# Kernel optimization log

Measured on AMD Instinct MI355X. Metric: run time of the kernel, lower is better.

Reference implementation:

```python
import jax, jax.numpy as jnp
import numpy as np
import math

TOTAL_RANK = 16
ACTIVE_RANK = 8
HADAMARD_DIM = 16
ADAPT_DIM = 32
HIDDEN = 2048
LN_EPS = 1e-5


def _hadamard(n: int) -> np.ndarray:
    # Replicates the module's recursive construction (normalizes by sqrt(n) at EVERY level).
    if n == 1:
        return np.array([[1.0]], dtype=np.float32)
    h = _hadamard(n // 2)
    return (np.block([[h, h], [h, -h]]) / math.sqrt(n)).astype(np.float32)


def setup_inputs() -> dict:
    key = jax.random.key(0)
    ks = jax.random.split(key, 8)
    B, S = 8, 4096
    hidden_states = jax.random.normal(ks[0], (B, S, HIDDEN), dtype=jnp.float32)
    rank_activations = jax.random.normal(ks[1], (B, S, TOTAL_RANK), dtype=jnp.float32)
    W1 = jax.random.normal(ks[2], (HIDDEN, ADAPT_DIM), dtype=jnp.float32) / math.sqrt(HIDDEN)
    b1 = jnp.zeros((ADAPT_DIM,), dtype=jnp.float32)
    ln_gamma = jnp.ones((ADAPT_DIM,), dtype=jnp.float32)
    ln_beta = jnp.zeros((ADAPT_DIM,), dtype=jnp.float32)
    W2 = jax.random.normal(ks[3], (ADAPT_DIM, TOTAL_RANK), dtype=jnp.float32) / math.sqrt(ADAPT_DIM)
    b2 = jnp.zeros((TOTAL_RANK,), dtype=jnp.float32)
    mask_logits = jax.random.normal(ks[4], (TOTAL_RANK,), dtype=jnp.float32) * 0.1
    rank_scales = jnp.ones((TOTAL_RANK,), dtype=jnp.float32)
    return {
        "hidden_states": hidden_states,
        "rank_activations": rank_activations,
        "W1": W1, "b1": b1, "ln_gamma": ln_gamma, "ln_beta": ln_beta,
        "W2": W2, "b2": b2, "mask_logits": mask_logits, "rank_scales": rank_scales,
    }


def reference(hidden_states, rank_activations, W1, b1, ln_gamma, ln_beta, W2, b2,
              mask_logits, rank_scales):
    B = hidden_states.shape[0]
    # Instance-adaptive logits: adaptation_net(hidden.mean(dim=1)) — eval mode (dropout off).
    pooled = jnp.mean(hidden_states, axis=1)                      # [B, H]
    x = pooled @ W1 + b1                                          # [B, A]
    mu = jnp.mean(x, axis=-1, keepdims=True)
    var = jnp.var(x, axis=-1, keepdims=True)
    x = (x - mu) * jax.lax.rsqrt(var + LN_EPS) * ln_gamma + ln_beta
    x = jax.nn.gelu(x, approximate=False)
    instance_logits = x @ W2 + b2                                 # [B, R]
    combined = instance_logits + mask_logits[None, :]
    # k-hot mask via top-k + scatter (eval path)
    _, idx = jax.lax.top_k(combined, ACTIVE_RANK)                 # [B, k]
    mask = jnp.zeros_like(combined).at[jnp.arange(B)[:, None], idx].set(1.0)
    # mask + scale
    scaled = rank_activations * mask[:, None, :] * rank_scales[None, None, :]  # [B,S,R]
    # Hadamard path: total_rank == hadamard_dim == 16 -> no padding, slice is no-op.
    H = jnp.asarray(_hadamard(HADAMARD_DIM))
    transformed = jnp.einsum('bsr,dr->bsd', scaled, H)            # x @ H.T
    final = transformed[:, :, :TOTAL_RANK]
    return final
```

## Files before the change

kernel.cpp:

```cpp
#include <hip/hip_runtime.h>
#include <hip/hip_bf16.h>
#include <math.h>

#define S_LEN   4096
#define HID     2048
#define NB      8
#define SC      128
#define S_PER   (S_LEN / SC)
#define R       16
#define AD      32

typedef float f4 __attribute__((ext_vector_type(4)));

__global__ void pool_proj(const float* __restrict__ hs,
                          const float* __restrict__ W1,
                          float* __restrict__ xpart) {
    __shared__ float hsum[HID];
    __shared__ float cpart[8][AD];
    int t  = threadIdx.x;
    int sc = blockIdx.x;
    int b  = blockIdx.y;

    const float* base = hs + ((size_t)b * S_LEN + (size_t)sc * S_PER) * HID;
    const f4* p0 = (const f4*)(base + t * 4);
    const f4* p1 = (const f4*)(base + 1024 + t * 4);
    f4 a0 = (f4)(0.f);
    f4 a1 = (f4)(0.f);
#pragma unroll 8
    for (int s = 0; s < S_PER; ++s) {
        f4 v0 = __builtin_nontemporal_load(p0 + (size_t)s * (HID / 4));
        f4 v1 = __builtin_nontemporal_load(p1 + (size_t)s * (HID / 4));
        a0 += v0;
        a1 += v1;
    }
    *(f4*)&hsum[t * 4]        = a0;
    *(f4*)&hsum[1024 + t * 4] = a1;
    __syncthreads();

    int j = t & 31, g = t >> 5;
    const float* w = W1 + (size_t)(g * 256) * AD + j;
    float c = 0.f;
#pragma unroll 4
    for (int k = 0; k < 256; ++k)
        c += hsum[g * 256 + k] * w[(size_t)k * AD];
    cpart[g][j] = c;
    __syncthreads();

    if (t < AD) {
        float s = 0.f;
#pragma unroll
        for (int gg = 0; gg < 8; ++gg) s += cpart[gg][t];
        xpart[((size_t)(b * SC + sc)) * AD + t] = s;
    }
}

__global__ void ctrl_hadamard(const float* __restrict__ xpart,
                              const float* __restrict__ b1,
                              const float* __restrict__ gamma,
                              const float* __restrict__ beta,
                              const float* __restrict__ W2,
                              const float* __restrict__ b2v,
                              const float* __restrict__ mlog,
                              const float* __restrict__ rsc,
                              const float* __restrict__ ra,
                              float* __restrict__ out) {
    __shared__ float xp[4][AD];
    __shared__ float xv[AD];
    __shared__ float xg[AD];
    __shared__ float comb[R];
    __shared__ float ms[R];
    int t   = threadIdx.x;
    int blk = blockIdx.x;
    int b   = blk >> 5;

    int j = t & 31, g = t >> 5;
    const float* xb = xpart + (size_t)b * SC * AD;
    float s = 0.f;
#pragma unroll 8
    for (int r = 0; r < 32; ++r) s += xb[(size_t)(g * 32 + r) * AD + j];
    xp[g][j] = s;
    __syncthreads();

    if (t < AD) {
        float x = 0.f;
#pragma unroll
        for (int gg = 0; gg < 4; ++gg) x += xp[gg][t];
        xv[t] = x * (1.0f / (float)S_LEN) + b1[t];
    }
    __syncthreads();

    if (t < AD) {
        float mu = 0.f;
#pragma unroll
        for (int k = 0; k < AD; ++k) mu += xv[k];
        mu *= (1.0f / AD);
        float var = 0.f;
#pragma unroll
        for (int k = 0; k < AD; ++k) { float d = xv[k] - mu; var += d * d; }
        var *= (1.0f / AD);
        float x = (xv[t] - mu) * rsqrtf(var + 1e-5f) * gamma[t] + beta[t];
        xg[t] = 0.5f * x * (1.0f + erff(x * 0.70710678118654752f));
    }
    __syncthreads();

    if (t < R) {
        float lg = b2v[t];
#pragma unroll
        for (int k = 0; k < AD; ++k) lg += xg[k] * W2[(size_t)k * R + t];
        comb[t] = lg + mlog[t];
    }
    __syncthreads();

    if (t < R) {
        float v = comb[t];
        int cnt = 0;
#pragma unroll
        for (int k = 0; k < R; ++k)
            cnt += (comb[k] > v) || (comb[k] == v && k < t);
        ms[t] = (cnt < 8) ? rsc[t] : 0.f;
    }
    __syncthreads();

    size_t row = (size_t)blk * 128 + t;
    const f4* src = (const f4*)(ra + row * R);
    float a[R];
#pragma unroll
    for (int i = 0; i < 4; ++i) {
        f4 v = __builtin_nontemporal_load(src + i);
        a[4 * i + 0] = v.x; a[4 * i + 1] = v.y;
        a[4 * i + 2] = v.z; a[4 * i + 3] = v.w;
    }
#pragma unroll
    for (int r = 0; r < R; ++r) a[r] *= ms[r];

#pragma unroll
    for (int hstep = 1; hstep < R; hstep <<= 1) {
#pragma unroll
        for (int i = 0; i < R; ++i) {
            if ((i & hstep) == 0) {
                float u = a[i], v = a[i | hstep];
                a[i] = u + v; a[i | hstep] = u - v;
            }
        }
    }

    f4* dst = (f4*)(out + row * R);
#pragma unroll
    for (int i = 0; i < 4; ++i) {
        f4 v;
        v.x = a[4 * i + 0] * 0.03125f; v.y = a[4 * i + 1] * 0.03125f;
        v.z = a[4 * i + 2] * 0.03125f; v.w = a[4 * i + 3] * 0.03125f;
        __builtin_nontemporal_store(v, dst + i);
    }
}

extern "C" void kernel_launch(void* const* d_in, const int* in_sizes, int n_in,
                              void* d_out, int out_size, void* d_ws, size_t ws_size,
                              hipStream_t stream) {
    const float* hs    = (const float*)d_in[0];
    const float* ra    = (const float*)d_in[1];
    const float* W1    = (const float*)d_in[2];
    const float* b1    = (const float*)d_in[3];
    const float* gamma = (const float*)d_in[4];
    const float* beta  = (const float*)d_in[5];
    const float* W2    = (const float*)d_in[6];
    const float* b2v   = (const float*)d_in[7];
    const float* mlog  = (const float*)d_in[8];
    const float* rsc   = (const float*)d_in[9];
    float* out = (float*)d_out;

    float* xpart = (float*)d_ws;

    pool_proj    <<<dim3(SC, NB), 256, 0, stream>>>(hs, W1, xpart);
    ctrl_hadamard<<<256, 128, 0, stream>>>(xpart, b1, gamma, beta,
                                           W2, b2v, mlog, rsc, ra, out);
}
```

Measured before the change: 56.85 us.

## Fuse pooling and controller/Hadamard into one cooperative kernel with grid sync

Merges the two kernels into a single cooperative launch of 1024 blocks. A grid-wide sync separates the pooled projection partials from the per-batch controller and the Hadamard stage. Each block then redoes the small controller computation and transforms 32 rows using only one wave. This is meant to remove the second launch and the gap between kernels. In exchange it adds grid-sync cost, requires all 1024 blocks to be co-resident, and leaves most threads idle in the Hadamard phase.

```diff
diff --git a/kernel.cpp b/kernel.cpp
--- a/kernel.cpp
+++ b/kernel.cpp
@@ -1,4 +1,5 @@
 #include <hip/hip_runtime.h>
+#include <hip/hip_cooperative_groups.h>
 #include <hip/hip_bf16.h>
 #include <math.h>
 
@@ -12,145 +13,152 @@
 
 typedef float f4 __attribute__((ext_vector_type(4)));
 
-__global__ void pool_proj(const float* __restrict__ hs,
-                          const float* __restrict__ W1,
-                          float* __restrict__ xpart) {
+namespace cg = cooperative_groups;
+
+__global__ __launch_bounds__(256, 4)
+void fused_all(const float* __restrict__ hs,
+               const float* __restrict__ W1,
+               const float* __restrict__ b1,
+               const float* __restrict__ gamma,
+               const float* __restrict__ beta,
+               const float* __restrict__ W2,
+               const float* __restrict__ b2v,
+               const float* __restrict__ mlog,
+               const float* __restrict__ rsc,
+               const float* __restrict__ ra,
+               float* __restrict__ xpart,
+               float* __restrict__ out) {
     __shared__ float hsum[HID];
-    __shared__ float cpart[8][AD];
-    int t  = threadIdx.x;
-    int sc = blockIdx.x;
-    int b  = blockIdx.y;
-
-    const float* base = hs + ((size_t)b * S_LEN + (size_t)sc * S_PER) * HID;
-    const f4* p0 = (const f4*)(base + t * 4);
-    const f4* p1 = (const f4*)(base + 1024 + t * 4);
-    f4 a0 = (f4)(0.f);
-    f4 a1 = (f4)(0.f);
-#pragma unroll 8
-    for (int s = 0; s < S_PER; ++s) {
-        f4 v0 = __builtin_nontemporal_load(p0 + (size_t)s * (HID / 4));
-        f4 v1 = __builtin_nontemporal_load(p1 + (size_t)s * (HID / 4));
-        a0 += v0;
-        a1 += v1;
-    }
-    *(f4*)&hsum[t * 4]        = a0;
-    *(f4*)&hsum[1024 + t * 4] = a1;
-    __syncthreads();
-
-    int j = t & 31, g = t >> 5;
-    const float* w = W1 + (size_t)(g * 256) * AD + j;
-    float c = 0.f;
-#pragma unroll 4
-    for (int k = 0; k < 256; ++k)
-        c += hsum[g * 256 + k] * w[(size_t)k * AD];
-    cpart[g][j] = c;
-    __syncthreads();
-
-    if (t < AD) {
-        float s = 0.f;
-#pragma unroll
-        for (int gg = 0; gg < 8; ++gg) s += cpart[gg][t];
-        xpart[((size_t)(b * SC + sc)) * AD + t] = s;
-    }
-}
-
-__global__ void ctrl_hadamard(const float* __restrict__ xpart,
-                              const float* __restrict__ b1,
-                              const float* __restrict__ gamma,
-                              const float* __restrict__ beta,
-                              const float* __restrict__ W2,
-                              const float* __restrict__ b2v,
-                              const float* __restrict__ mlog,
-                              const float* __restrict__ rsc,
-                              const float* __restrict__ ra,
-                              float* __restrict__ out) {
-    __shared__ float xp[4][AD];
+    __shared__ float gp[8][AD];
     __shared__ float xv[AD];
     __shared__ float xg[AD];
     __shared__ float comb[R];
     __shared__ float ms[R];
+
     int t   = threadIdx.x;
     int blk = blockIdx.x;
-    int b   = blk >> 5;
+    int b   = blk >> 7;
 
-    int j = t & 31, g = t >> 5;
-    const float* xb = xpart + (size_t)b * SC * AD;
-    float s = 0.f;
+    {
+        int sc = blk & (SC - 1);
+        const float* base = hs + ((size_t)b * S_LEN + (size_t)sc * S_PER) * HID;
+        const f4* p0 = (const f4*)(base + t * 4);
+        const f4* p1 = (const f4*)(base + 1024 + t * 4);
+        f4 a0 = (f4)(0.f);
+        f4 a1 = (f4)(0.f);
 #pragma unroll 8
-    for (int r = 0; r < 32; ++r) s += xb[(size_t)(g * 32 + r) * AD + j];
-    xp[g][j] = s;
-    __syncthreads();
+        for (int s = 0; s < S_PER; ++s) {
+            f4 v0 = __builtin_nontemporal_load(p0 + (size_t)s * (HID / 4));
+            f4 v1 = __builtin_nontemporal_load(p1 + (size_t)s * (HID / 4));
+            a0 += v0;
+            a1 += v1;
+        }
+        *(f4*)&hsum[t * 4]        = a0;
+        *(f4*)&hsum[1024 + t * 4] = a1;
+        __syncthreads();
 
-    if (t < AD) {
-        float x = 0.f;
+        int j = t & 31, g = t >> 5;
+        const float* w = W1 + (size_t)(g * 256) * AD + j;
+        float c = 0.f;
+#pragma unroll 4
+        for (int k = 0; k < 256; ++k)
+            c += hsum[g * 256 + k] * w[(size_t)k * AD];
+        gp[g][j] = c;
+        __syncthreads();
+
+        if (t < AD) {
+            float s = 0.f;
 #pragma unroll
-        for (int gg = 0; gg < 4; ++gg) x += xp[gg][t];
-        xv[t] = x * (1.0f / (float)S_LEN) + b1[t];
-    }
-    __syncthreads();
-
-    if (t < AD) {
-        float mu = 0.f;
-#pragma unroll
-        for (int k = 0; k < AD; ++k) mu += xv[k];
-        mu *= (1.0f / AD);
-        float var = 0.f;
-#pragma unroll
-        for (int k = 0; k < AD; ++k) { float d = xv[k] - mu; var += d * d; }
-        var *= (1.0f / AD);
-        float x = (xv[t] - mu) * rsqrtf(var + 1e-5f) * gamma[t] + beta[t];
-        xg[t] = 0.5f * x * (1.0f + erff(x * 0.70710678118654752f));
-    }
-    __syncthreads();
-
-    if (t < R) {
-        float lg = b2v[t];
-#pragma unroll
-        for (int k = 0; k < AD; ++k) lg += xg[k] * W2[(size_t)k * R + t];
-        comb[t] = lg + mlog[t];
-    }
-    __syncthreads();
-
-    if (t < R) {
-        float v = comb[t];
-        int cnt = 0;
-#pragma unroll
-        for (int k = 0; k < R; ++k)
-            cnt += (comb[k] > v) || (comb[k] == v && k < t);
-        ms[t] = (cnt < 8) ? rsc[t] : 0.f;
-    }
-    __syncthreads();
-
-    size_t row = (size_t)blk * 128 + t;
-    const f4* src = (const f4*)(ra + row * R);
-    float a[R];
-#pragma unroll
-    for (int i = 0; i < 4; ++i) {
-        f4 v = __builtin_nontemporal_load(src + i);
-        a[4 * i + 0] = v.x; a[4 * i + 1] = v.y;
-        a[4 * i + 2] = v.z; a[4 * i + 3] = v.w;
-    }
-#pragma unroll
-    for (int r = 0; r < R; ++r) a[r] *= ms[r];
-
-#pragma unroll
-    for (int hstep = 1; hstep < R; hstep <<= 1) {
-#pragma unroll
-        for (int i = 0; i < R; ++i) {
-            if ((i & hstep) == 0) {
-                float u = a[i], v = a[i | hstep];
-                a[i] = u + v; a[i | hstep] = u - v;
-            }
+            for (int gg = 0; gg < 8; ++gg) s += gp[gg][t];
+            xpart[((size_t)blk) * AD + t] = s;
         }
     }
 
-    f4* dst = (f4*)(out + row * R);
+    cg::this_grid().sync();
+
+    {
+        int j = t & 31, g = t >> 5;
+        const float* xb = xpart + (size_t)b * SC * AD;
+        float s = 0.f;
+#pragma unroll 4
+        for (int r = 0; r < 16; ++r)
+            s += xb[(size_t)(g * 16 + r) * AD + j];
+        gp[g][j] = s;
+        __syncthreads();
+
+        if (t < AD) {
+            float x = 0.f;
 #pragma unroll
-    for (int i = 0; i < 4; ++i) {
-        f4 v;
-        v.x = a[4 * i + 0] * 0.03125f; v.y = a[4 * i + 1] * 0.03125f;
-        v.z = a[4 * i + 2] * 0.03125f; v.w = a[4 * i + 3] * 0.03125f;
-        __builtin_nontemporal_store(v, dst + i);
+            for (int gg = 0; gg < 8; ++gg) x += gp[gg][t];
+            xv[t] = x * (1.0f / (float)S_LEN) + b1[t];
+        }
+        __syncthreads();
+
+        if (t < AD) {
+            float mu = 0.f;
+#pragma unroll
+            for (int k = 0; k < AD; ++k) mu += xv[k];
+            mu *= (1.0f / AD);
+            float var = 0.f;
+#pragma unroll
+            for (int k = 0; k < AD; ++k) { float d = xv[k] - mu; var += d * d; }
+            var *= (1.0f / AD);
+            float x = (xv[t] - mu) * rsqrtf(var + 1e-5f) * gamma[t] + beta[t];
+            xg[t] = 0.5f * x * (1.0f + erff(x * 0.70710678118654752f));
+        }
+        __syncthreads();
+
+        if (t < R) {
+            float lg = b2v[t];
+#pragma unroll
+            for (int k = 0; k < AD; ++k) lg += xg[k] * W2[(size_t)k * R + t];
+            comb[t] = lg + mlog[t];
+        }
+        __syncthreads();
+
+        if (t < R) {
+            float v = comb[t];
+            int cnt = 0;
+#pragma unroll
+            for (int k = 0; k < R; ++k)
+                cnt += (comb[k] > v) || (comb[k] == v && k < t);
+            ms[t] = (cnt < 8) ? rsc[t] : 0.f;
+        }
+        __syncthreads();
+    }
+
+    if (t < 32) {
+        size_t row = (size_t)blk * 32 + t;
+        const f4* src = (const f4*)(ra + row * R);
+        float a[R];
+#pragma unroll
+        for (int i = 0; i < 4; ++i) {
+            f4 v = __builtin_nontemporal_load(src + i);
+            a[4 * i + 0] = v.x; a[4 * i + 1] = v.y;
+            a[4 * i + 2] = v.z; a[4 * i + 3] = v.w;
+        }
+#pragma unroll
+        for (int r = 0; r < R; ++r) a[r] *= ms[r];
+
+#pragma unroll
+        for (int hstep = 1; hstep < R; hstep <<= 1) {
+#pragma unroll
+            for (int i = 0; i < R; ++i) {
+                if ((i & hstep) == 0) {
+                    float u = a[i], v = a[i | hstep];
+                    a[i] = u + v; a[i | hstep] = u - v;
+                }
+            }
+        }
+
+        f4* dst = (f4*)(out + row * R);
+#pragma unroll
+        for (int i = 0; i < 4; ++i) {
+            f4 v;
+            v.x = a[4 * i + 0] * 0.03125f; v.y = a[4 * i + 1] * 0.03125f;
+            v.z = a[4 * i + 2] * 0.03125f; v.w = a[4 * i + 3] * 0.03125f;
+            __builtin_nontemporal_store(v, dst + i);
+        }
     }
 }
 
@@ -167,11 +175,14 @@
     const float* b2v   = (const float*)d_in[7];
     const float* mlog  = (const float*)d_in[8];
     const float* rsc   = (const float*)d_in[9];
-    float* out = (float*)d_out;
-
+    float* out   = (float*)d_out;
     float* xpart = (float*)d_ws;
 
-    pool_proj    <<<dim3(SC, NB), 256, 0, stream>>>(hs, W1, xpart);
-    ctrl_hadamard<<<256, 128, 0, stream>>>(xpart, b1, gamma, beta,
-                                           W2, b2v, mlog, rsc, ra, out);
+    void* args[] = {
+        (void*)&hs, (void*)&W1, (void*)&b1, (void*)&gamma, (void*)&beta,
+        (void*)&W2, (void*)&b2v, (void*)&mlog, (void*)&rsc, (void*)&ra,
+        (void*)&xpart, (void*)&out
+    };
+    hipLaunchCooperativeKernel((void*)fused_all, dim3(NB * SC), dim3(256),
+                               args, 0, stream);
 }
```

After: 202.9 us. 3.57x slower.

## Replace shared-memory controller stages with per-wave shuffle reductions

Applied to the files above, without the earlier changes.

Rewrites the per-block controller (pooled sum, LayerNorm, GELU, W2 projection, top-k mask) so each 64-lane wave computes it redundantly with cross-lane shuffles, removing the shared-memory stages and block barriers. The output scale of 1/32 is folded into the mask values, and the rank_activations load becomes a regular rather than nontemporal load. This cuts serial latency before the streaming Hadamard part, at the cost of some redundant arithmetic per wave.

```diff
diff --git a/kernel.cpp b/kernel.cpp
--- a/kernel.cpp
+++ b/kernel.cpp
@@ -64,74 +64,92 @@
                               const float* __restrict__ rsc,
                               const float* __restrict__ ra,
                               float* __restrict__ out) {
-    __shared__ float xp[4][AD];
-    __shared__ float xv[AD];
-    __shared__ float xg[AD];
-    __shared__ float comb[R];
-    __shared__ float ms[R];
     int t   = threadIdx.x;
     int blk = blockIdx.x;
     int b   = blk >> 5;
+    int lane = t & 63;
+    int j    = lane & 31;
+    int half = lane >> 5;
 
-    int j = t & 31, g = t >> 5;
-    const float* xb = xpart + (size_t)b * SC * AD;
+    const float* xb = xpart + ((size_t)b * SC + half * 64) * AD + j;
     float s = 0.f;
 #pragma unroll 8
-    for (int r = 0; r < 32; ++r) s += xb[(size_t)(g * 32 + r) * AD + j];
-    xp[g][j] = s;
-    __syncthreads();
+    for (int r = 0; r < 64; ++r) s += xb[(size_t)r * AD];
+    s += __shfl_xor(s, 32);
 
-    if (t < AD) {
-        float x = 0.f;
+    float xv = s * (1.0f / (float)S_LEN) + b1[j];
+
+    float m = xv;
 #pragma unroll
-        for (int gg = 0; gg < 4; ++gg) x += xp[gg][t];
-        xv[t] = x * (1.0f / (float)S_LEN) + b1[t];
+    for (int d = 1; d < 64; d <<= 1) m += __shfl_xor(m, d);
+    float mu = m * (1.0f / 64.0f);
+    float dv = xv - mu;
+    float vs = dv * dv;
+#pragma unroll
+    for (int d = 1; d < 64; d <<= 1) vs += __shfl_xor(vs, d);
+    float var = vs * (1.0f / 64.0f);
+
+    float xln = dv * rsqrtf(var + 1e-5f) * gamma[j] + beta[j];
+    float xg  = 0.5f * xln * (1.0f + erff(xln * 0.70710678118654752f));
+
+    float p[8];
+#pragma unroll
+    for (int kk = 0; kk < 8; ++kk)
+        p[kk] = xg * W2[(size_t)j * R + half * 8 + kk];
+#pragma unroll
+    for (int d = 1; d < 32; d <<= 1) {
+#pragma unroll
+        for (int kk = 0; kk < 8; ++kk) p[kk] += __shfl_xor(p[kk], d);
     }
-    __syncthreads();
+#pragma unroll
+    for (int kk = 0; kk < 8; ++kk)
+        p[kk] += b2v[half * 8 + kk] + mlog[half * 8 + kk];
 
-    if (t < AD) {
-        float mu = 0.f;
+    float q[8];
 #pragma unroll
-        for (int k = 0; k < AD; ++k) mu += xv[k];
-        mu *= (1.0f / AD);
-        float var = 0.f;
+    for (int kk = 0; kk < 8; ++kk) q[kk] = __shfl_xor(p[kk], 32);
+    float lo[8], hi[8];
 #pragma unroll
-        for (int k = 0; k < AD; ++k) { float d = xv[k] - mu; var += d * d; }
-        var *= (1.0f / AD);
-        float x = (xv[t] - mu) * rsqrtf(var + 1e-5f) * gamma[t] + beta[t];
-        xg[t] = 0.5f * x * (1.0f + erff(x * 0.70710678118654752f));
+    for (int kk = 0; kk < 8; ++kk) {
+        lo[kk] = (half == 0) ? p[kk] : q[kk];
+        hi[kk] = (half == 0) ? q[kk] : p[kk];
     }
-    __syncthreads();
 
-    if (t < R) {
-        float lg = b2v[t];
+    float msv[R];
 #pragma unroll
-        for (int k = 0; k < AD; ++k) lg += xg[k] * W2[(size_t)k * R + t];
-        comb[t] = lg + mlog[t];
-    }
-    __syncthreads();
-
-    if (t < R) {
-        float v = comb[t];
+    for (int k = 0; k < 8; ++k) {
+        float v = lo[k];
         int cnt = 0;
 #pragma unroll
-        for (int k = 0; k < R; ++k)
-            cnt += (comb[k] > v) || (comb[k] == v && k < t);
-        ms[t] = (cnt < 8) ? rsc[t] : 0.f;
+        for (int m2 = 0; m2 < 8; ++m2) {
+            cnt += (lo[m2] > v) || (lo[m2] == v && m2 < k);
+            cnt += (hi[m2] > v);
+        }
+        msv[k] = (cnt < 8) ? rsc[k] * 0.03125f : 0.f;
     }
-    __syncthreads();
+#pragma unroll
+    for (int k = 0; k < 8; ++k) {
+        float v = hi[k];
+        int cnt = 0;
+#pragma unroll
+        for (int m2 = 0; m2 < 8; ++m2) {
+            cnt += (lo[m2] > v) || (lo[m2] == v);
+            cnt += (hi[m2] > v) || (hi[m2] == v && m2 < k);
+        }
+        msv[8 + k] = (cnt < 8) ? rsc[8 + k] * 0.03125f : 0.f;
+    }
 
     size_t row = (size_t)blk * 128 + t;
     const f4* src = (const f4*)(ra + row * R);
     float a[R];
 #pragma unroll
     for (int i = 0; i < 4; ++i) {
-        f4 v = __builtin_nontemporal_load(src + i);
+        f4 v = src[i];
         a[4 * i + 0] = v.x; a[4 * i + 1] = v.y;
         a[4 * i + 2] = v.z; a[4 * i + 3] = v.w;
     }
 #pragma unroll
-    for (int r = 0; r < R; ++r) a[r] *= ms[r];
+    for (int r = 0; r < R; ++r) a[r] *= msv[r];
 
 #pragma unroll
     for (int hstep = 1; hstep < R; hstep <<= 1) {
@@ -148,8 +166,8 @@
 #pragma unroll
     for (int i = 0; i < 4; ++i) {
         f4 v;
-        v.x = a[4 * i + 0] * 0.03125f; v.y = a[4 * i + 1] * 0.03125f;
-        v.z = a[4 * i + 2] * 0.03125f; v.w = a[4 * i + 3] * 0.03125f;
+        v.x = a[4 * i + 0]; v.y = a[4 * i + 1];
+        v.z = a[4 * i + 2]; v.w = a[4 * i + 3];
         __builtin_nontemporal_store(v, dst + i);
     }
 }
```

After: 60.46 us. 1.06x slower.

## Move controller MLP into last-arriving pool block via atomic counter

Applied to the files above, without the earlier changes.

Instead of every Hadamard block redundantly reducing 128 partials and running LayerNorm, GELU, the W2 projection and top-k, the last pool_proj block per batch (found through an atomic counter) does this once and writes a per-batch mask with the 1/32 scale folded in. The Hadamard kernel then only loads 16 mask values and uses 256-thread blocks. This adds a memset launch and a threadfence/atomic handshake, and the tail block runs serially after the last arrival.

```diff
diff --git a/kernel.cpp b/kernel.cpp
--- a/kernel.cpp
+++ b/kernel.cpp
@@ -14,9 +14,22 @@
 
 __global__ void pool_proj(const float* __restrict__ hs,
                           const float* __restrict__ W1,
-                          float* __restrict__ xpart) {
+                          const float* __restrict__ b1,
+                          const float* __restrict__ gamma,
+                          const float* __restrict__ beta,
+                          const float* __restrict__ W2,
+                          const float* __restrict__ b2v,
+                          const float* __restrict__ mlog,
+                          const float* __restrict__ rsc,
+                          float* __restrict__ xpart,
+                          float* __restrict__ msout,
+                          int* __restrict__ cnt) {
     __shared__ float hsum[HID];
     __shared__ float cpart[8][AD];
+    __shared__ float xv[AD];
+    __shared__ float xg[AD];
+    __shared__ float comb[R];
+    __shared__ int   iswin;
     int t  = threadIdx.x;
     int sc = blockIdx.x;
     int b  = blockIdx.y;
@@ -52,40 +65,36 @@
         for (int gg = 0; gg < 8; ++gg) s += cpart[gg][t];
         xpart[((size_t)(b * SC + sc)) * AD + t] = s;
     }
-}
-
-__global__ void ctrl_hadamard(const float* __restrict__ xpart,
-                              const float* __restrict__ b1,
-                              const float* __restrict__ gamma,
-                              const float* __restrict__ beta,
-                              const float* __restrict__ W2,
-                              const float* __restrict__ b2v,
-                              const float* __restrict__ mlog,
-                              const float* __restrict__ rsc,
-                              const float* __restrict__ ra,
-                              float* __restrict__ out) {
-    __shared__ float xp[4][AD];
-    __shared__ float xv[AD];
-    __shared__ float xg[AD];
-    __shared__ float comb[R];
-    __shared__ float ms[R];
-    int t   = threadIdx.x;
-    int blk = blockIdx.x;
-    int b   = blk >> 5;
-
-    int j = t & 31, g = t >> 5;
-    const float* xb = xpart + (size_t)b * SC * AD;
-    float s = 0.f;
-#pragma unroll 8
-    for (int r = 0; r < 32; ++r) s += xb[(size_t)(g * 32 + r) * AD + j];
-    xp[g][j] = s;
-    __syncthreads();
-
-    if (t < AD) {
-        float x = 0.f;
-#pragma unroll
-        for (int gg = 0; gg < 4; ++gg) x += xp[gg][t];
-        xv[t] = x * (1.0f / (float)S_LEN) + b1[t];
+
+    if (t == 0) {
+        __threadfence();
+        int old = atomicAdd(&cnt[b], 1);
+        iswin = (old == SC - 1);
+        if (iswin) __threadfence();
+    }
+    __syncthreads();
+    if (!iswin) return;
+
+    {
+        f4* red = (f4*)hsum;
+        const f4* xp4 = (const f4*)(xpart + (size_t)b * SC * AD);
+        int c4 = t & 7, rg = t >> 3;
+        f4 acc = (f4)(0.f);
+#pragma unroll
+        for (int r = 0; r < 4; ++r)
+            acc += xp4[(size_t)(rg + r * 32) * 8 + c4];
+        red[rg * 8 + c4] = acc;
+    }
+    __syncthreads();
+    if (t < 8) {
+        f4* red = (f4*)hsum;
+        f4 s = (f4)(0.f);
+#pragma unroll
+        for (int rg = 0; rg < 32; ++rg) s += red[rg * 8 + t];
+        xv[t * 4 + 0] = s.x * (1.0f / (float)S_LEN) + b1[t * 4 + 0];
+        xv[t * 4 + 1] = s.y * (1.0f / (float)S_LEN) + b1[t * 4 + 1];
+        xv[t * 4 + 2] = s.z * (1.0f / (float)S_LEN) + b1[t * 4 + 2];
+        xv[t * 4 + 3] = s.w * (1.0f / (float)S_LEN) + b1[t * 4 + 3];
     }
     __syncthreads();
 
@@ -113,15 +122,25 @@
 
     if (t < R) {
         float v = comb[t];
-        int cnt = 0;
+        int cn = 0;
 #pragma unroll
         for (int k = 0; k < R; ++k)
-            cnt += (comb[k] > v) || (comb[k] == v && k < t);
-        ms[t] = (cnt < 8) ? rsc[t] : 0.f;
-    }
-    __syncthreads();
-
-    size_t row = (size_t)blk * 128 + t;
+            cn += (comb[k] > v) || (comb[k] == v && k < t);
+        msout[b * R + t] = (cn < 8) ? rsc[t] * 0.03125f : 0.f;
+    }
+}
+
+__global__ void apply_hadamard(const float* __restrict__ msout,
+                               const float* __restrict__ ra,
+                               float* __restrict__ out) {
+    __shared__ float ms[R];
+    int t   = threadIdx.x;
+    int blk = blockIdx.x;
+    int b   = blk >> 4;
+    if (t < R) ms[t] = msout[b * R + t];
+    __syncthreads();
+
+    size_t row = (size_t)blk * 256 + t;
     const f4* src = (const f4*)(ra + row * R);
     float a[R];
 #pragma unroll
@@ -148,8 +167,8 @@
 #pragma unroll
     for (int i = 0; i < 4; ++i) {
         f4 v;
-        v.x = a[4 * i + 0] * 0.03125f; v.y = a[4 * i + 1] * 0.03125f;
-        v.z = a[4 * i + 2] * 0.03125f; v.w = a[4 * i + 3] * 0.03125f;
+        v.x = a[4 * i + 0]; v.y = a[4 * i + 1];
+        v.z = a[4 * i + 2]; v.w = a[4 * i + 3];
         __builtin_nontemporal_store(v, dst + i);
     }
 }
@@ -170,8 +189,12 @@
     float* out = (float*)d_out;
 
     float* xpart = (float*)d_ws;
-
-    pool_proj    <<<dim3(SC, NB), 256, 0, stream>>>(hs, W1, xpart);
-    ctrl_hadamard<<<256, 128, 0, stream>>>(xpart, b1, gamma, beta,
-                                           W2, b2v, mlog, rsc, ra, out);
+    float* msout = xpart + (size_t)NB * SC * AD;
+    int*   cnt   = (int*)(msout + NB * R);
+
+    hipMemsetAsync(cnt, 0, NB * sizeof(int), stream);
+    pool_proj     <<<dim3(SC, NB), 256, 0, stream>>>(hs, W1, b1, gamma, beta,
+                                                     W2, b2v, mlog, rsc,
+                                                     xpart, msout, cnt);
+    apply_hadamard<<<128, 256, 0, stream>>>(msout, ra, out);
 }
```

Result: slower. 80.89 us (+42.3%).
